# Performance work log

Hardware: AMD Instinct MI355X
Metric: run time of the kernel (lower is better)

## Reference

```python
import jax, jax.numpy as jnp
import numpy as np

L, D, H, FF = 4, 512, 8, 2048
B, S = 32, 512
DK = D // H
EPS = 1e-5


def setup_inputs() -> dict:
    key = jax.random.key(0)
    ks = iter(jax.random.split(key, 20))
    r = lambda *sh: 0.02 * jax.random.normal(next(ks), sh, dtype=jnp.float32)
    inp = {
        "src": jax.random.normal(next(ks), (B, S, D), dtype=jnp.float32),
        "Wq": r(L, D, D), "bq": jnp.zeros((L, D), jnp.float32),
        "Wk": r(L, D, D), "bk": jnp.zeros((L, D), jnp.float32),
        "Wv": r(L, D, D), "bv": jnp.zeros((L, D), jnp.float32),
        "Wo": r(L, D, D), "bo": jnp.zeros((L, D), jnp.float32),
        "ln1_g": jnp.ones((L, D), jnp.float32), "ln1_b": jnp.zeros((L, D), jnp.float32),
        "ln2_g": jnp.ones((L, D), jnp.float32), "ln2_b": jnp.zeros((L, D), jnp.float32),
        "Wf1": r(L, D, FF), "bf1": jnp.zeros((L, FF), jnp.float32),
        "Wf2": r(L, FF, D), "bf2": jnp.zeros((L, D), jnp.float32),
    }
    return inp


def _ln(x, g, b):
    m = jnp.mean(x, -1, keepdims=True)
    v = jnp.mean(jnp.square(x - m), -1, keepdims=True)
    return (x - m) * jax.lax.rsqrt(v + EPS) * g + b


def reference(src, Wq, bq, Wk, bk, Wv, bv, Wo, bo,
              ln1_g, ln1_b, ln2_g, ln2_b, Wf1, bf1, Wf2, bf2):
    b, s, d = src.shape
    scale = DK ** -0.5
    x = src
    scores = None  # residual attention: raw pre-softmax scores carried across layers
    for i in range(L):
        q = (jnp.einsum('bsd,de->bse', x, Wq[i]) + bq[i]).reshape(b, s, H, DK)
        k = (jnp.einsum('bsd,de->bse', x, Wk[i]) + bk[i]).reshape(b, s, H, DK)
        v = (jnp.einsum('bsd,de->bse', x, Wv[i]) + bv[i]).reshape(b, s, H, DK)
        attn_scores = jnp.einsum('bqhd,bkhd->bhqk', q, k) * scale  # [B,H,S,S]
        if scores is not None:
            attn_scores = attn_scores + scores
        scores = attn_scores
        w = jax.nn.softmax(attn_scores, axis=-1)
        o = jnp.einsum('bhqk,bkhd->bqhd', w, v).reshape(b, s, d)
        o = jnp.einsum('bsd,de->bse', o, Wo[i]) + bo[i]
        x = _ln(x + o, ln1_g[i], ln1_b[i])  # post-norm
        h = jax.nn.gelu(jnp.einsum('bsd,df->bsf', x, Wf1[i]) + bf1[i], approximate=False)
        ff = jnp.einsum('bsf,fd->bsd', h, Wf2[i]) + bf2[i]
        x = _ln(x + ff, ln2_g[i], ln2_b[i])
    return x
```

## Files before the change

### kernel.cpp

```cpp
#include <hip/hip_runtime.h>
#include <hip/hip_bf16.h>


#define NL 4
#define DMODEL 512
#define NH 8
#define FFDIM 2048
#define BATCH 32
#define SEQ 512
#define DHEAD 64
#define NTOK (BATCH*SEQ)
#define LDQKV (3*DMODEL)

typedef unsigned short u16;
typedef __bf16 bf16x8 __attribute__((ext_vector_type(8)));
typedef float f32x4 __attribute__((ext_vector_type(4)));
typedef unsigned short u16x8 __attribute__((ext_vector_type(8)));
typedef unsigned short u16x4 __attribute__((ext_vector_type(4)));

__device__ __forceinline__ u16 f2b(float f){
  return __builtin_bit_cast(u16, (__bf16)f);
}
__device__ __forceinline__ float b2f(u16 h){
  return __builtin_bit_cast(float, ((unsigned)h)<<16);
}
__device__ __forceinline__ void gll16(const void* g, void* l){
  __builtin_amdgcn_global_load_lds((__attribute__((address_space(1))) void*)(g),
                                   (__attribute__((address_space(3))) void*)(l), 16, 0, 0);
}
__device__ __forceinline__ float wred_sum(float v){
  #pragma unroll
  for (int off=32; off; off>>=1) v += __shfl_xor(v, off, 64);
  return v;
}
__device__ __forceinline__ float gelu_f(float v){
  float y = 0.79788456080286536f*(v + 0.044715f*v*v*v);
  float t = __expf(2.0f*y);
  return v - v/(t + 1.0f);
}

template<int OUT_MODE>
__global__ __launch_bounds__(256) void gemm_bt(
    const u16* __restrict__ A, const u16* __restrict__ Bt,
    const float* __restrict__ bias, u16* __restrict__ Cout,
    int M, int N, int K)
{
  __shared__ u16 smem[16384];
  const int t = threadIdx.x;
  const int w = t>>6, lane = t&63;

  const int gx = gridDim.x;
  const int id = blockIdx.y*gx + blockIdx.x;
  const int cpx = (gx*gridDim.y) >> 3;
  const int nid = (id & 7)*cpx + (id >> 3);
  const int m0 = (nid / gx)*128, n0 = (nid % gx)*128;

  const int wr = (w>>1)*64, wc = (w&1)*64;

  f32x4 acc[4][4];
  #pragma unroll
  for (int m=0;m<4;m++)
    #pragma unroll
    for (int n=0;n<4;n++) acc[m][n] = f32x4{0.f,0.f,0.f,0.f};

  const int srow = t>>2;
  const int scol = (((t&3) ^ ((srow>>1)&3)))*8;
  const size_t aBase = (size_t)(m0 + srow)*K + scol;
  const size_t bBase = (size_t)(n0 + srow)*K + scol;
  const size_t rstep = (size_t)64*K;
  const int dstw = w*512;

  #define STAGE(buf, k0) do{                                       \
    u16* base_ = smem + (buf)*8192;                                \
    gll16(A  + aBase + (k0),          base_ + dstw);               \
    gll16(A  + aBase + rstep + (k0),  base_ + 2048 + dstw);        \
    gll16(Bt + bBase + (k0),          base_ + 4096 + dstw);        \
    gll16(Bt + bBase + rstep + (k0),  base_ + 6144 + dstw);        \
  }while(0)

  const int g = lane>>4, r16 = lane&15;
  const int chunkoff = ((g ^ ((r16>>1)&3))<<3);

  STAGE(0, 0);
  int cur = 0;
  for (int k0=0; k0<K; k0+=32){
    if (k0+32 < K){
      STAGE(cur^1, k0+32);
      asm volatile("s_waitcnt vmcnt(4)" ::: "memory");
    } else {
      asm volatile("s_waitcnt vmcnt(0)" ::: "memory");
    }
    asm volatile("s_barrier" ::: "memory");
    const u16* lA = smem + cur*8192;
    const u16* lB = lA + 4096;
    bf16x8 af[4], bfr[4];
    #pragma unroll
    for (int m=0;m<4;m++) af[m]  = *(const bf16x8*)(lA + (wr+m*16+r16)*32 + chunkoff);
    #pragma unroll
    for (int n=0;n<4;n++) bfr[n] = *(const bf16x8*)(lB + (wc+n*16+r16)*32 + chunkoff);
    #pragma unroll
    for (int m=0;m<4;m++)
      #pragma unroll
      for (int n=0;n<4;n++)
        acc[m][n] = __builtin_amdgcn_mfma_f32_16x16x32_bf16(af[m], bfr[n], acc[m][n], 0,0,0);
    asm volatile("s_waitcnt lgkmcnt(0)" ::: "memory");
    asm volatile("s_barrier" ::: "memory");
    cur ^= 1;
  }
  #undef STAGE

  const int c16 = lane&15, r4 = (lane>>4)*4;
  float bb[4];
  #pragma unroll
  for (int n=0;n<4;n++) bb[n] = bias[n0 + wc + n*16 + c16];
  #pragma unroll
  for (int s=0;s<2;s++){
    __syncthreads();
    if ((w>>1)==s){
      #pragma unroll
      for (int m=0;m<4;m++)
        #pragma unroll
        for (int n=0;n<4;n++)
          #pragma unroll
          for (int j=0;j<4;j++){
            float val = acc[m][n][j] + bb[n];
            if (OUT_MODE==2) val = gelu_f(val);
            const int row = m*16 + r4 + j;
            const int col = (wc + n*16 + c16) ^ (((row>>2)&3)<<4);
            smem[row*128 + col] = f2b(val);
          }
    }
    __syncthreads();
    #pragma unroll
    for (int i=0;i<4;i++){
      const int lrow = i*16 + (t>>4), colr = (t&15)*8;
      u16x8 vv = *(const u16x8*)(smem + lrow*128 + (colr ^ (((lrow>>2)&3)<<4)));
      *(u16x8*)(Cout + (size_t)(m0 + s*64 + lrow)*N + n0 + colr) = vv;
    }
  }
}

template<int OUT_MODE>
__global__ __launch_bounds__(512) void gemm_bt_wide(
    const u16* __restrict__ A, const u16* __restrict__ Bt,
    const float* __restrict__ bias, u16* __restrict__ Cout,
    int M, int N, int K)
{
  __shared__ u16 smem[24576];
  const int t = threadIdx.x;
  const int w = t>>6, lane = t&63;

  const int gx = gridDim.x;
  const int id = blockIdx.y*gx + blockIdx.x;
  const int cpx = (gx*gridDim.y) >> 3;
  const int nid = (id & 7)*cpx + (id >> 3);
  const int m0 = (nid / gx)*128, n0 = (nid % gx)*256;

  const int wr = (w>>2)*64, wc = (w&3)*64;

  f32x4 acc[4][4];
  #pragma unroll
  for (int m=0;m<4;m++)
    #pragma unroll
    for (int n=0;n<4;n++) acc[m][n] = f32x4{0.f,0.f,0.f,0.f};

  const int srow = t>>2;
  const int scol = (((t&3) ^ ((srow>>1)&3)))*8;
  const size_t aBase = (size_t)(m0 + srow)*K + scol;
  const size_t bBase = (size_t)(n0 + srow)*K + scol;
  const size_t brstep = (size_t)128*K;
  const int dstw = w*512;

  #define STAGEW(buf, k0) do{                                      \
    u16* base_ = smem + (buf)*12288;                               \
    gll16(A  + aBase + (k0),           base_ + dstw);              \
    gll16(Bt + bBase + (k0),           base_ + 4096 + dstw);       \
    gll16(Bt + bBase + brstep + (k0),  base_ + 8192 + dstw);       \
  }while(0)

  const int g = lane>>4, r16 = lane&15;
  const int chunkoff = ((g ^ ((r16>>1)&3))<<3);

  STAGEW(0, 0);
  int cur = 0;
  for (int k0=0; k0<K; k0+=32){
    if (k0+32 < K){
      STAGEW(cur^1, k0+32);
      asm volatile("s_waitcnt vmcnt(3)" ::: "memory");
    } else {
      asm volatile("s_waitcnt vmcnt(0)" ::: "memory");
    }
    asm volatile("s_barrier" ::: "memory");
    const u16* lA = smem + cur*12288;
    const u16* lB = lA + 4096;
    bf16x8 af[4], bfr[4];
    #pragma unroll
    for (int m=0;m<4;m++) af[m]  = *(const bf16x8*)(lA + (wr+m*16+r16)*32 + chunkoff);
    #pragma unroll
    for (int n=0;n<4;n++) bfr[n] = *(const bf16x8*)(lB + (wc+n*16+r16)*32 + chunkoff);
    #pragma unroll
    for (int m=0;m<4;m++)
      #pragma unroll
      for (int n=0;n<4;n++)
        acc[m][n] = __builtin_amdgcn_mfma_f32_16x16x32_bf16(af[m], bfr[n], acc[m][n], 0,0,0);
    asm volatile("s_waitcnt lgkmcnt(0)" ::: "memory");
    asm volatile("s_barrier" ::: "memory");
    cur ^= 1;
  }
  #undef STAGEW

  const int c16 = lane&15, r4 = (lane>>4)*4;
  float bb[4];
  #pragma unroll
  for (int n=0;n<4;n++) bb[n] = bias[n0 + wc + n*16 + c16];
  #pragma unroll
  for (int s=0;s<2;s++){
    __syncthreads();
    if ((w>>2)==s){
      #pragma unroll
      for (int m=0;m<4;m++)
        #pragma unroll
        for (int n=0;n<4;n++)
          #pragma unroll
          for (int j=0;j<4;j++){
            float val = acc[m][n][j] + bb[n];
            if (OUT_MODE==2) val = gelu_f(val);
            const int row = m*16 + r4 + j;
            const int col = (wc + n*16 + c16) ^ (((row>>2)&3)<<4);
            smem[row*256 + col] = f2b(val);
          }
    }
    __syncthreads();
    #pragma unroll
    for (int i=0;i<4;i++){
      const int lrow = i*16 + (t>>5), colr = (t&31)*8;
      u16x8 vv = *(const u16x8*)(smem + lrow*256 + (colr ^ (((lrow>>2)&3)<<4)));
      *(u16x8*)(Cout + (size_t)(m0 + s*64 + lrow)*N + n0 + colr) = vv;
    }
  }
}

__global__ __launch_bounds__(256) void transpose_v(
    const u16* __restrict__ qkv, u16* __restrict__ vt)
{
  __shared__ u16 T[64*33];
  const int t = threadIdx.x;
  const int s0 = blockIdx.x*32;
  const int bh = blockIdx.y;
  const int b = bh >> 3, h = bh & 7;
  const u16* v = qkv + 2*DMODEL + h*DHEAD;
  #pragma unroll
  for (int i=0;i<8;i++){
    int idx = i*256 + t;
    int sl = idx >> 6, d = idx & 63;
    T[d*33 + sl] = v[(size_t)(b*SEQ + s0 + sl)*LDQKV + d];
  }
  __syncthreads();
  u16* o = vt + (size_t)bh*DHEAD*SEQ;
  #pragma unroll
  for (int i=0;i<8;i++){
    int idx = i*256 + t;
    int d = idx >> 5, sl = idx & 31;
    o[(size_t)d*SEQ + s0 + sl] = T[d*33 + sl];
  }
}

template<int ADDP, int WRITES>
__global__ __launch_bounds__(256) void fused_attn(
    const u16* __restrict__ qkv, const u16* __restrict__ vt,
    u16* __restrict__ sc, u16* __restrict__ outp)
{
  __shared__ u16 smem[20480];
  u16* lQ = smem;
  const int t=threadIdx.x, w=t>>6, lane=t&63;
  const int g = lane>>4, r16 = lane&15;

  const int dd = blockIdx.x;
  const int c  = dd&7;
  const int j_ = dd>>3;
  const int qb = j_&7;
  const int bh = (j_>>3)*8 + c;
  const int b = bh>>3, h = bh&7;
  const int q0 = qb*64;

  const int srow = t>>3;
  const int schunk = (t&7) ^ (srow&7);
  const u16* qp = qkv + h*DHEAD;
  const u16* kp = qkv + DMODEL + h*DHEAD;
  const size_t qBase = (size_t)(b*SEQ + q0 + srow)*LDQKV + (size_t)(schunk*8);
  const size_t kRow0 = (size_t)(b*SEQ + srow)*LDQKV + (size_t)(schunk*8);

  #pragma unroll
  for (int r=0;r<2;r++)
    gll16(qp + qBase + (size_t)(r*32)*LDQKV, lQ + r*2048 + w*512);
  #pragma unroll
  for (int r=0;r<4;r++)
    gll16(kp + kRow0 + (size_t)(r*32)*LDQKV, smem + 4096 + r*2048 + w*512);
  __syncthreads();

  u16* sblk = sc + ((((size_t)bh*8 + qb)*4)*4 + w)*2048 + lane*4;
  const u16* vtp = vt + (size_t)bh*DHEAD*SEQ;

  bf16x8 ones;
  #pragma unroll
  for (int j=0;j<8;j++) ones[j] = (__bf16)1.0f;

  f32x4 pvacc[4][4], rs[4];
  #pragma unroll
  for (int nf=0;nf<4;nf++){
    rs[nf] = f32x4{0.f,0.f,0.f,0.f};
    #pragma unroll
    for (int nd=0;nd<4;nd++) pvacc[nf][nd] = f32x4{0.f,0.f,0.f,0.f};
  }

  #pragma unroll
  for (int kt=0; kt<4; kt++){
    const int cur = 4096 + (kt&1)*8192;
    const int nxt = 4096 + ((kt+1)&1)*8192;
    const int ktw = kt*128 + w*32;
    u16* skt = sblk + (size_t)kt*16384;

    u16x4 sold[2][4];
    if (ADDP){
      #pragma unroll
      for (int mf=0;mf<2;mf++)
        #pragma unroll
        for (int nf=0;nf<4;nf++)
          sold[mf][nf] = *(const u16x4*)(skt + (mf*4+nf)*256);
    }
    u16x4 vfrag[4][2];
    #pragma unroll
    for (int nd=0;nd<4;nd++){
      const u16* vr = vtp + (size_t)(nd*16+r16)*SEQ + ktw + g*4;
      vfrag[nd][0] = *(const u16x4*)(vr);
      vfrag[nd][1] = *(const u16x4*)(vr + 16);
    }
    if (kt<3){
      const size_t kB = kRow0 + (size_t)((kt+1)*128)*LDQKV;
      #pragma unroll
      for (int r=0;r<4;r++)
        gll16(kp + kB + (size_t)(r*32)*LDQKV, smem + nxt + r*2048 + w*512);
    }

    f32x4 acc[2][4];
    #pragma unroll
    for (int mf=0;mf<2;mf++)
      #pragma unroll
      for (int nf=0;nf<4;nf++) acc[mf][nf] = f32x4{0.f,0.f,0.f,0.f};
    #pragma unroll
    for (int ks=0; ks<2; ks++){
      bf16x8 af[2], bfq[4];
      #pragma unroll
      for (int mf=0;mf<2;mf++){
        const int row = w*32 + mf*16 + r16;
        af[mf] = *(const bf16x8*)(smem + cur + row*64 + (((ks*4+g)^(row&7))<<3));
      }
      #pragma unroll
      for (int nf=0;nf<4;nf++){
        const int row = nf*16 + r16;
        bfq[nf] = *(const bf16x8*)(lQ + row*64 + (((ks*4+g)^(row&7))<<3));
      }
      #pragma unroll
      for (int mf=0;mf<2;mf++)
        #pragma unroll
        for (int nf=0;nf<4;nf++)
          acc[mf][nf] = __builtin_amdgcn_mfma_f32_16x16x32_bf16(af[mf], bfq[nf], acc[mf][nf], 0,0,0);
    }

    bf16x8 pe[4];
    #pragma unroll
    for (int nf=0;nf<4;nf++){
      u16x8 pk;
      #pragma unroll
      for (int mf=0;mf<2;mf++){
        float v[4]; u16x4 sn;
        #pragma unroll
        for (int j=0;j<4;j++){
          v[j] = acc[mf][nf][j]*0.125f;
          if (ADDP) v[j] += b2f(sold[mf][nf][j]);
          if (WRITES) sn[j] = f2b(v[j]);
          pk[mf*4+j] = f2b(__expf(v[j]));
        }
        if (WRITES)
          *(u16x4*)(skt + (mf*4+nf)*256) = sn;
      }
      pe[nf] = __builtin_bit_cast(bf16x8, pk);
      rs[nf] = __builtin_amdgcn_mfma_f32_16x16x32_bf16(pe[nf], ones, rs[nf], 0,0,0);
    }

    #pragma unroll
    for (int nd=0;nd<4;nd++){
      u16x8 vv;
      #pragma unroll
      for (int j=0;j<4;j++){ vv[j] = vfrag[nd][0][j]; vv[4+j] = vfrag[nd][1][j]; }
      bf16x8 vb = __builtin_bit_cast(bf16x8, vv);
      #pragma unroll
      for (int nf=0;nf<4;nf++)
        pvacc[nf][nd] = __builtin_amdgcn_mfma_f32_16x16x32_bf16(pe[nf], vb, pvacc[nf][nd], 0,0,0);
    }

    __syncthreads();
  }

  float* bufA = (float*)smem;
  float* bufB = bufA + 64*68;
  float* bufR = bufB + 64*68;
  if (r16 == 0){
    #pragma unroll
    for (int nf=0;nf<4;nf++)
      #pragma unroll
      for (int j=0;j<4;j++)
        bufR[w*64 + nf*16 + g*4 + j] = rs[nf][j];
  }
  if (w < 2){
    float* dst = (w==0) ? bufA : bufB;
    #pragma unroll
    for (int nf=0;nf<4;nf++)
      #pragma unroll
      for (int nd=0;nd<4;nd++)
        #pragma unroll
        for (int j=0;j<4;j++)
          dst[(nf*16+g*4+j)*68 + nd*16+r16] = pvacc[nf][nd][j];
  }
  __syncthreads();
  if (w >= 2){
    float* dst = (w==2) ? bufA : bufB;
    #pragma unroll
    for (int nf=0;nf<4;nf++)
      #pragma unroll
      for (int nd=0;nd<4;nd++)
        #pragma unroll
        for (int j=0;j<4;j++)
          dst[(nf*16+g*4+j)*68 + nd*16+r16] += pvacc[nf][nd][j];
  }
  __syncthreads();
  {
    const int q = t>>2, db = (t&3)*16;
    const float tot = bufR[q] + bufR[64+q] + bufR[128+q] + bufR[192+q];
    const float inv = 1.0f/tot;
    const float* ra = bufA + q*68 + db;
    const float* rb = bufB + q*68 + db;
    u16* ob = outp + ((size_t)(b*SEQ + q0 + q)*NH + h)*DHEAD + db;
    u16x8 o0, o1;
    #pragma unroll
    for (int j=0;j<8;j++) o0[j] = f2b((ra[j]   + rb[j]  )*inv);
    #pragma unroll
    for (int j=0;j<8;j++) o1[j] = f2b((ra[8+j] + rb[8+j])*inv);
    *(u16x8*)(ob)     = o0;
    *(u16x8*)(ob + 8) = o1;
  }
}

template<int WF>
__global__ __launch_bounds__(256) void ln_k(
    const u16* __restrict__ xin, const u16* __restrict__ proj,
    const float* __restrict__ g, const float* __restrict__ beta,
    u16* __restrict__ xb, float* __restrict__ fout)
{
  const int row = blockIdx.x*4 + (threadIdx.x>>6);
  const int lane = threadIdx.x & 63;
  const size_t base = (size_t)row*DMODEL + lane*8;
  u16x8 a = *(const u16x8*)(xin + base);
  u16x8 p = *(const u16x8*)(proj + base);
  float v[8];
  #pragma unroll
  for (int j=0;j<8;j++) v[j] = b2f(a[j]) + b2f(p[j]);
  float s = 0.f;
  #pragma unroll
  for (int j=0;j<8;j++) s += v[j];
  s = wred_sum(s);
  const float mean = s * (1.0f/DMODEL);
  float qv = 0.f;
  #pragma unroll
  for (int j=0;j<8;j++){ float d = v[j]-mean; qv += d*d; }
  qv = wred_sum(qv);
  const float rstd = rsqrtf(qv*(1.0f/DMODEL) + 1e-5f);
  const int c = lane*8;
  float o[8]; u16x8 ob;
  #pragma unroll
  for (int j=0;j<8;j++){
    o[j] = (v[j]-mean)*rstd*g[c+j] + beta[c+j];
    ob[j] = f2b(o[j]);
  }
  *(u16x8*)(xb + base) = ob;
  if (WF){
    *(float4*)(fout + base)     = make_float4(o[0],o[1],o[2],o[3]);
    *(float4*)(fout + base + 4) = make_float4(o[4],o[5],o[6],o[7]);
  }
}

__global__ __launch_bounds__(256) void wt_conv(
    const float* __restrict__ Win, u16* __restrict__ Wout,
    int K, int N, long outLstride)
{
  __shared__ float T[32][33];
  const int t = threadIdx.x;
  const int tx = t&31, ty = t>>5;
  const int n0 = blockIdx.x*32, k0 = blockIdx.y*32, l = blockIdx.z;
  const float* W = Win + (size_t)l*K*N;
  u16* O = Wout + (size_t)l*outLstride;
  #pragma unroll
  for (int i=0;i<4;i++)
    T[ty+i*8][tx] = W[(size_t)(k0+ty+i*8)*N + n0 + tx];
  __syncthreads();
  #pragma unroll
  for (int i=0;i<4;i++){
    const int nn = ty + i*8;
    O[(size_t)(n0+nn)*K + k0 + tx] = f2b(T[tx][nn]);
  }
}

__global__ void bias_concat(const float* __restrict__ bq, const float* __restrict__ bk,
                            const float* __restrict__ bv, float* __restrict__ out)
{
  const int i = blockIdx.x*256 + threadIdx.x;
  if (i >= NL*LDQKV) return;
  const int l = i / LDQKV, c = i % LDQKV;
  float v;
  if (c < DMODEL)        v = bq[l*DMODEL + c];
  else if (c < 2*DMODEL) v = bk[l*DMODEL + c - DMODEL];
  else                   v = bv[l*DMODEL + c - 2*DMODEL];
  out[i] = v;
}

__global__ void conv_src(const float* __restrict__ src, u16* __restrict__ xb)
{
  const int i = blockIdx.x*256 + threadIdx.x;
  float4 v = ((const float4*)src)[i];
  u16x4 bb; bb[0]=f2b(v.x); bb[1]=f2b(v.y); bb[2]=f2b(v.z); bb[3]=f2b(v.w);
  *(u16x4*)(xb + (size_t)i*4) = bb;
}

__global__ void diag_fill(float* __restrict__ o, int n, float v){
  int i = blockIdx.x*256 + threadIdx.x;
  if (i < n) o[i] = v;
}

extern "C" void kernel_launch(void* const* d_in, const int* in_sizes, int n_in,
                              void* d_out, int out_size, void* d_ws, size_t ws_size,
                              hipStream_t stream)
{
  (void)in_sizes; (void)n_in;
  const float* src = (const float*)d_in[0];
  const float* Wq  = (const float*)d_in[1];
  const float* bq  = (const float*)d_in[2];
  const float* Wk  = (const float*)d_in[3];
  const float* bk  = (const float*)d_in[4];
  const float* Wv  = (const float*)d_in[5];
  const float* bv  = (const float*)d_in[6];
  const float* Wo  = (const float*)d_in[7];
  const float* bo  = (const float*)d_in[8];
  const float* ln1g= (const float*)d_in[9];
  const float* ln1b= (const float*)d_in[10];
  const float* ln2g= (const float*)d_in[11];
  const float* ln2b= (const float*)d_in[12];
  const float* Wf1 = (const float*)d_in[13];
  const float* bf1 = (const float*)d_in[14];
  const float* Wf2 = (const float*)d_in[15];
  const float* bf2 = (const float*)d_in[16];

  const size_t NEEDED = 260071424ull;
  if (ws_size < NEEDED){
    diag_fill<<<(out_size+255)/256, 256, 0, stream>>>((float*)d_out, out_size,
                                                      (float)(ws_size >> 20));
    return;
  }
  char* ws = (char*)d_ws;
  u16*  xb     = (u16*)(ws + 0);
  u16*  qkv    = (u16*)(ws + 16777216);
  u16*  attn_o = (u16*)(ws + 16777216);
  u16*  hbuf   = (u16*)(ws + 16777216);
  u16*  vt     = (u16*)(ws + 67108864);
  u16*  scores = (u16*)(ws + 83886080);
  u16*  proj   = (u16*)(ws + 218103808);
  u16*  wqkvT  = (u16*)(ws + 234881024);
  u16*  woT    = (u16*)(ws + 241172480);
  u16*  wf1T   = (u16*)(ws + 243269632);
  u16*  wf2T   = (u16*)(ws + 251658240);
  float* qkvb  = (float*)(ws + 260046848);

  dim3 blk(256);
  dim3 blkw(512);

  wt_conv<<<dim3(16,16,4),blk,0,stream>>>(Wq, wqkvT,                  DMODEL, DMODEL, (long)LDQKV*DMODEL);
  wt_conv<<<dim3(16,16,4),blk,0,stream>>>(Wk, wqkvT + DMODEL*DMODEL,  DMODEL, DMODEL, (long)LDQKV*DMODEL);
  wt_conv<<<dim3(16,16,4),blk,0,stream>>>(Wv, wqkvT + 2*DMODEL*DMODEL,DMODEL, DMODEL, (long)LDQKV*DMODEL);
  wt_conv<<<dim3(16,16,4),blk,0,stream>>>(Wo, woT,  DMODEL, DMODEL, (long)DMODEL*DMODEL);
  wt_conv<<<dim3(64,16,4),blk,0,stream>>>(Wf1, wf1T, DMODEL, FFDIM, (long)FFDIM*DMODEL);
  wt_conv<<<dim3(16,64,4),blk,0,stream>>>(Wf2, wf2T, FFDIM, DMODEL, (long)DMODEL*FFDIM);
  bias_concat<<<24,blk,0,stream>>>(bq,bk,bv,qkvb);
  conv_src<<<8192,blk,0,stream>>>(src, xb);

  for (int l=0; l<NL; l++){
    gemm_bt_wide<0><<<dim3(6,128),blkw,0,stream>>>(xb, wqkvT + (size_t)l*LDQKV*DMODEL,
                                                   qkvb + l*LDQKV, qkv, NTOK, LDQKV, DMODEL);
    transpose_v<<<dim3(16,BATCH*NH),blk,0,stream>>>(qkv, vt);
    if (l==0)
      fused_attn<0,1><<<dim3(2048),blk,0,stream>>>(qkv, vt, scores, attn_o);
    else if (l<NL-1)
      fused_attn<1,1><<<dim3(2048),blk,0,stream>>>(qkv, vt, scores, attn_o);
    else
      fused_attn<1,0><<<dim3(2048),blk,0,stream>>>(qkv, vt, scores, attn_o);
    gemm_bt<0><<<dim3(4,128),blk,0,stream>>>(attn_o, woT + (size_t)l*DMODEL*DMODEL,
                                             bo + l*DMODEL, proj, NTOK, DMODEL, DMODEL);
    ln_k<0><<<NTOK/4,blk,0,stream>>>(xb, proj, ln1g + l*DMODEL, ln1b + l*DMODEL, xb, nullptr);
    gemm_bt_wide<2><<<dim3(8,128),blkw,0,stream>>>(xb, wf1T + (size_t)l*FFDIM*DMODEL,
                                                   bf1 + l*FFDIM, hbuf, NTOK, FFDIM, DMODEL);
    gemm_bt<0><<<dim3(4,128),blk,0,stream>>>(hbuf, wf2T + (size_t)l*DMODEL*FFDIM,
                                             bf2 + l*DMODEL, proj, NTOK, DMODEL, FFDIM);
    if (l==NL-1)
      ln_k<1><<<NTOK/4,blk,0,stream>>>(xb, proj, ln2g + l*DMODEL, ln2b + l*DMODEL, xb, (float*)d_out);
    else
      ln_k<0><<<NTOK/4,blk,0,stream>>>(xb, proj, ln2g + l*DMODEL, ln2b + l*DMODEL, xb, nullptr);
  }
}
```

Measured before the change: 999.1 us.

## Fuse V transpose into QKV GEMM epilogue and relax attention loop barrier

The QKV GEMM epilogue now writes the V columns directly in transposed per-head layout, which removes the separate transpose_v kernel and its extra read/write pass over V. In the attention kernel, the end-of-iteration __syncthreads is replaced by explicit waitcnt instructions plus s_barrier, so outstanding score-write stores are not fully drained before the barrier, and a sched_barrier is added after the K prefetch. The transposed epilogue does strided 8-element gathers from shared memory, which may cause bank conflicts. The hand-tuned vmcnt count assumes a fixed number of outstanding memory operations.

Measured after the change: 1.007 ms. Within noise of the previous version (+0.8%).

```diff
diff --git a/kernel.cpp b/kernel.cpp
--- a/kernel.cpp
+++ b/kernel.cpp
@@ -144,6 +144,7 @@
 __global__ __launch_bounds__(512) void gemm_bt_wide(
     const u16* __restrict__ A, const u16* __restrict__ Bt,
     const float* __restrict__ bias, u16* __restrict__ Cout,
+    u16* __restrict__ vtout,
     int M, int N, int K)
 {
   __shared__ u16 smem[24576];
@@ -231,37 +232,30 @@
           }
     }
     __syncthreads();
-    #pragma unroll
-    for (int i=0;i<4;i++){
-      const int lrow = i*16 + (t>>5), colr = (t&31)*8;
-      u16x8 vv = *(const u16x8*)(smem + lrow*256 + (colr ^ (((lrow>>2)&3)<<4)));
-      *(u16x8*)(Cout + (size_t)(m0 + s*64 + lrow)*N + n0 + colr) = vv;
-    }
-  }
-}
-
-__global__ __launch_bounds__(256) void transpose_v(
-    const u16* __restrict__ qkv, u16* __restrict__ vt)
-{
-  __shared__ u16 T[64*33];
-  const int t = threadIdx.x;
-  const int s0 = blockIdx.x*32;
-  const int bh = blockIdx.y;
-  const int b = bh >> 3, h = bh & 7;
-  const u16* v = qkv + 2*DMODEL + h*DHEAD;
-  #pragma unroll
-  for (int i=0;i<8;i++){
-    int idx = i*256 + t;
-    int sl = idx >> 6, d = idx & 63;
-    T[d*33 + sl] = v[(size_t)(b*SEQ + s0 + sl)*LDQKV + d];
-  }
-  __syncthreads();
-  u16* o = vt + (size_t)bh*DHEAD*SEQ;
-  #pragma unroll
-  for (int i=0;i<8;i++){
-    int idx = i*256 + t;
-    int d = idx >> 5, sl = idx & 31;
-    o[(size_t)d*SEQ + s0 + sl] = T[d*33 + sl];
+    if (OUT_MODE==3 && n0 >= 1024){
+      const int b_    = (m0 + s*64) >> 9;
+      const int sbase = (m0 + s*64) & 511;
+      const int f = t & 255, half = t >> 8;
+      const int fg = (n0 - 1024) + f;
+      u16* vrow = vtout + (((size_t)(b_*NH + (fg>>6)))*DHEAD + (fg&63))*SEQ + sbase + half*32;
+      #pragma unroll
+      for (int cth=0; cth<4; cth++){
+        u16x8 val;
+        #pragma unroll
+        for (int j=0;j<8;j++){
+          const int row = half*32 + cth*8 + j;
+          val[j] = smem[row*256 + (f ^ (((row>>2)&3)<<4))];
+        }
+        *(u16x8*)(vrow + cth*8) = val;
+      }
+    } else {
+      #pragma unroll
+      for (int i=0;i<4;i++){
+        const int lrow = i*16 + (t>>5), colr = (t&31)*8;
+        u16x8 vv = *(const u16x8*)(smem + lrow*256 + (colr ^ (((lrow>>2)&3)<<4)));
+        *(u16x8*)(Cout + (size_t)(m0 + s*64 + lrow)*N + n0 + colr) = vv;
+      }
+    }
   }
 }
 
@@ -341,6 +335,7 @@
       for (int r=0;r<4;r++)
         gll16(kp + kB + (size_t)(r*32)*LDQKV, smem + nxt + r*2048 + w*512);
     }
+    __builtin_amdgcn_sched_barrier(0);
 
     f32x4 acc[2][4];
     #pragma unroll
@@ -399,7 +394,12 @@
         pvacc[nf][nd] = __builtin_amdgcn_mfma_f32_16x16x32_bf16(pe[nf], vb, pvacc[nf][nd], 0,0,0);
     }
 
-    __syncthreads();
+    asm volatile("s_waitcnt lgkmcnt(0)" ::: "memory");
+    if (kt<3){
+      if (WRITES) asm volatile("s_waitcnt vmcnt(8)" ::: "memory");
+      else        asm volatile("s_waitcnt vmcnt(0)" ::: "memory");
+    }
+    asm volatile("s_barrier" ::: "memory");
   }
 
   float* bufA = (float*)smem;
@@ -592,9 +592,8 @@
   conv_src<<<8192,blk,0,stream>>>(src, xb);
 
   for (int l=0; l<NL; l++){
-    gemm_bt_wide<0><<<dim3(6,128),blkw,0,stream>>>(xb, wqkvT + (size_t)l*LDQKV*DMODEL,
-                                                   qkvb + l*LDQKV, qkv, NTOK, LDQKV, DMODEL);
-    transpose_v<<<dim3(16,BATCH*NH),blk,0,stream>>>(qkv, vt);
+    gemm_bt_wide<3><<<dim3(6,128),blkw,0,stream>>>(xb, wqkvT + (size_t)l*LDQKV*DMODEL,
+                                                   qkvb + l*LDQKV, qkv, vt, NTOK, LDQKV, DMODEL);
     if (l==0)
       fused_attn<0,1><<<dim3(2048),blk,0,stream>>>(qkv, vt, scores, attn_o);
     else if (l<NL-1)
@@ -605,7 +604,7 @@
                                              bo + l*DMODEL, proj, NTOK, DMODEL, DMODEL);
     ln_k<0><<<NTOK/4,blk,0,stream>>>(xb, proj, ln1g + l*DMODEL, ln1b + l*DMODEL, xb, nullptr);
     gemm_bt_wide<2><<<dim3(8,128),blkw,0,stream>>>(xb, wf1T + (size_t)l*FFDIM*DMODEL,
-                                                   bf1 + l*FFDIM, hbuf, NTOK, FFDIM, DMODEL);
+                                                   bf1 + l*FFDIM, hbuf, nullptr, NTOK, FFDIM, DMODEL);
     gemm_bt<0><<<dim3(4,128),blk,0,stream>>>(hbuf, wf2T + (size_t)l*DMODEL*FFDIM,
                                              bf2 + l*DMODEL, proj, NTOK, DMODEL, FFDIM);
     if (l==NL-1)
```
